# Optimization experiments

Hardware: AMD Instinct MI355X
Metric: run time of the kernel (lower is better)

## Reference

```python
import jax, jax.numpy as jnp
import numpy as np


def setup_inputs() -> dict:
    key = jax.random.key(0)
    ks = jax.random.split(key, 8)
    B, A = 2048, 64
    STATE, ACT = 5, 4
    d_in = STATE + ACT  # 9
    x = jax.random.normal(ks[0], (B, STATE), dtype=jnp.float32)
    actions = jax.random.normal(ks[1], (A, ACT), dtype=jnp.float32)
    def lin(k, fin, fout):
        return jax.random.normal(k, (fin, fout), dtype=jnp.float32) / np.sqrt(fin)
    W1 = lin(ks[2], d_in, 128); b1 = jnp.zeros((128,), jnp.float32)
    W2 = lin(ks[3], 128, 1024); b2 = jnp.zeros((1024,), jnp.float32)
    W3 = lin(ks[4], 1024, 1024); b3 = jnp.zeros((1024,), jnp.float32)
    W4 = lin(ks[5], 1024, 128); b4 = jnp.zeros((128,), jnp.float32)
    W5 = lin(ks[6], 128, 1); b5 = jnp.zeros((1,), jnp.float32)
    return {"x": x, "actions": actions,
            "W1": W1, "b1": b1, "W2": W2, "b2": b2, "W3": W3, "b3": b3,
            "W4": W4, "b4": b4, "W5": W5, "b5": b5}


def reference(x, actions, W1, b1, W2, b2, W3, b3, W4, b4, W5, b5):
    # x: [B,5] states; actions: [A,4] candidate actions.
    # Equivalent to the original's per-sample per-action loop: evaluate the
    # 5-layer Tanh MLP on concat(state, action) for every (sample, action) pair.
    B = x.shape[0]
    A = actions.shape[0]
    s = jnp.broadcast_to(x[:, None, :], (B, A, x.shape[1]))
    a = jnp.broadcast_to(actions[None, :, :], (B, A, actions.shape[1]))
    inp = jnp.concatenate([s, a], axis=-1)  # [B,A,9]
    h = jnp.tanh(inp @ W1 + b1)
    h = jnp.tanh(h @ W2 + b2)
    h = jnp.tanh(h @ W3 + b3)
    h = jnp.tanh(h @ W4 + b4)
    values = (h @ W5 + b5)[..., 0]  # [B,A]
    best = jnp.argmax(values, axis=1)  # [B]
    max_value_action = actions[best]  # [B,4]
    return (max_value_action, values)
```

## Files before the change

kernel.cpp:

```cpp
#include <hip/hip_runtime.h>
#include <hip/hip_bf16.h>
#include <math.h>


typedef short bf16x8 __attribute__((ext_vector_type(8)));
typedef float f32x4 __attribute__((ext_vector_type(4)));
typedef float f32x16 __attribute__((ext_vector_type(16)));

__device__ __host__ inline unsigned short f2bf(float f) {
    union { float f; unsigned u; } v; v.f = f;
    unsigned r = v.u + 0x7fff + ((v.u >> 16) & 1);
    return (unsigned short)(r >> 16);
}
__device__ inline unsigned short cvt_bf16(float f) {
    __hip_bfloat16 h = __float2bfloat16(f);
    return *reinterpret_cast<unsigned short*>(&h);
}
__device__ inline float bf2f(unsigned short b) {
    union { unsigned u; float f; } v; v.u = ((unsigned)b) << 16;
    return v.f;
}
__device__ inline float fast_tanh(float x) {
    float e = __expf(2.0f * x);
    return 1.0f - 2.0f * __builtin_amdgcn_rcpf(e + 1.0f);
}

#define DELTA 0.025f
#define ITEM_CAP 16384

struct WLE { unsigned s, base, nc, pad; };

#define HSWZ(row, b) ((b) ^ (((row) & 15) << 4))

__global__ __launch_bounds__(256) void pack_all(
    const float* __restrict__ W2, const float* __restrict__ W3, const float* __restrict__ W4,
    unsigned short* __restrict__ W2p, unsigned short* __restrict__ W3p,
    unsigned short* __restrict__ W4p, unsigned* __restrict__ cnts)
{
    int tid = blockIdx.x * 256 + threadIdx.x;
    if (tid < 2) cnts[tid] = 0u;
    int blob = tid >> 6, lane = tid & 63;
    if (blob >= 2560) return;
    bf16x8 v;
    if (blob < 256) {
        int nt = blob >> 2, kt = blob & 3;
        int n = nt * 16 + (lane & 15);
        int kbase = kt * 32 + ((lane >> 4) & 3) * 8;
        #pragma unroll
        for (int e = 0; e < 8; ++e) v[e] = (short)f2bf(W2[(size_t)(kbase + e) * 1024 + n]);
        *(bf16x8*)&W2p[(size_t)blob * 512 + lane * 8] = v;
    } else if (blob < 2304) {
        int lb = blob - 256;
        int nt = lb >> 6, kt = lb & 63;
        int n = nt * 32 + (lane & 31);
        int kbase = kt * 16 + (lane >> 5) * 8;
        #pragma unroll
        for (int e = 0; e < 8; ++e) v[e] = (short)f2bf(W3[(size_t)(kbase + e) * 1024 + n]);
        *(bf16x8*)&W3p[(size_t)lb * 512 + lane * 8] = v;
    } else {
        int lb = blob - 2304;
        int nt = lb >> 5, kt = lb & 31;
        int n = nt * 16 + (lane & 15);
        int kbase = kt * 32 + ((lane >> 4) & 3) * 8;
        #pragma unroll
        for (int e = 0; e < 8; ++e) v[e] = (short)f2bf(W4[(size_t)(kbase + e) * 128 + n]);
        *(bf16x8*)&W4p[(size_t)lb * 512 + lane * 8] = v;
    }
}

__global__ __launch_bounds__(1024, 4) void qnet_mfma(
    const float* __restrict__ x, const float* __restrict__ actions,
    const float* __restrict__ W1, const float* __restrict__ b1,
    const float* __restrict__ b2, const float* __restrict__ b3,
    const float* __restrict__ b4,
    const float* __restrict__ W5, const float* __restrict__ b5,
    const unsigned short* __restrict__ W2p,
    const unsigned short* __restrict__ W3p,
    const unsigned short* __restrict__ W4p,
    float* __restrict__ values, float* __restrict__ out_actions,
    unsigned* __restrict__ cnts, WLE* __restrict__ wl,
    unsigned* __restrict__ items)
{
    __shared__ unsigned short h2b[2][64 * 256];
    __shared__ unsigned short hc[64 * 128];

    const int t = threadIdx.x;
    const int lane = t & 63;
    const int wave = t >> 6;
    const int grp = (wave >> 2) & 1;
    const int p0 = blockIdx.x * 64;
    const int l15 = lane & 15;
    const int kb16 = (lane >> 4) * 16;
    const int kb32 = (lane >> 5) * 16;

    {
        int r = t >> 4;
        int c0 = (t & 15) * 8;
        const float* xs = &x[blockIdx.x * 5];
        const float* as = &actions[r * 4];
        float in[9] = { xs[0], xs[1], xs[2], xs[3], xs[4], as[0], as[1], as[2], as[3] };
        #pragma unroll
        for (int j = 0; j < 8; ++j) {
            int c = c0 + j;
            float acc = b1[c];
            #pragma unroll
            for (int k = 0; k < 9; ++k) acc += in[k] * W1[k * 128 + c];
            *(unsigned short*)((char*)hc + r * 256 + HSWZ(r, c * 2)) = cvt_bf16(fast_tanh(acc));
        }
    }
    __syncthreads();

    auto layer2_chunk = [&](int c, int buf) {
        const int nT = c * 16 + wave;
        const float bv = b2[nT * 16 + l15];
        char* bufp = (char*)&h2b[buf][0];
        const int lcb = (wave * 16 + l15) * 2;
        #pragma unroll 1
        for (int rt = 0; rt < 4; ++rt) {
            f32x4 acc = (f32x4){ bv, bv, bv, bv };
            const int row = rt * 16 + l15;
            #pragma unroll
            for (int ks = 0; ks < 4; ++ks) {
                bf16x8 b = *(const bf16x8*)((const char*)W2p + (nT * 4 + ks) * 1024 + lane * 16);
                bf16x8 a = *(const bf16x8*)((const char*)hc + row * 256 + HSWZ(row, ks * 64 + kb16));
                acc = __builtin_amdgcn_mfma_f32_16x16x32_bf16(a, b, acc, 0, 0, 0);
            }
            #pragma unroll
            for (int rr = 0; rr < 4; ++rr) {
                int m = rt * 16 + (lane >> 4) * 4 + rr;
                *(unsigned short*)(bufp + m * 512 + HSWZ(m, lcb)) = cvt_bf16(fast_tanh(acc[rr]));
            }
        }
    };

    f32x16 a00, a01, a10, a11;
    {
        float bv0 = b3[wave * 64 + (lane & 31)];
        float bv1 = b3[wave * 64 + 32 + (lane & 31)];
        #pragma unroll
        for (int i = 0; i < 16; ++i) { a00[i] = bv0; a10[i] = bv0; a01[i] = bv1; a11[i] = bv1; }
    }
    const int r0 = lane & 31, r1 = 32 + (lane & 31);

    auto l3_step = [&](int c) {
        const char* bufp = (const char*)&h2b[c & 1][0];
        const char* bb = (const char*)W3p + (wave * 128 + c * 16) * 1024 + lane * 16;
        __builtin_amdgcn_s_setprio(1);
        #pragma unroll 2
        for (int kt = 0; kt < 16; ++kt) {
            bf16x8 A0 = *(const bf16x8*)(bufp + r0 * 512 + HSWZ(r0, kt * 32 + kb32));
            bf16x8 A1 = *(const bf16x8*)(bufp + r1 * 512 + HSWZ(r1, kt * 32 + kb32));
            bf16x8 B0 = *(const bf16x8*)(bb + kt * 1024);
            bf16x8 B1 = *(const bf16x8*)(bb + 65536 + kt * 1024);
            a00 = __builtin_amdgcn_mfma_f32_32x32x16_bf16(A0, B0, a00, 0, 0, 0);
            a10 = __builtin_amdgcn_mfma_f32_32x32x16_bf16(A1, B0, a10, 0, 0, 0);
            a01 = __builtin_amdgcn_mfma_f32_32x32x16_bf16(A0, B1, a01, 0, 0, 0);
            a11 = __builtin_amdgcn_mfma_f32_32x32x16_bf16(A1, B1, a11, 0, 0, 0);
        }
        __builtin_amdgcn_s_setprio(0);
    };

    layer2_chunk(0, 0);
    __syncthreads();

    for (int c = 0; c < 4; ++c) {
        if (grp == 0) {
            if (c < 3) layer2_chunk(c + 1, (c + 1) & 1);
            l3_step(c);
        } else {
            l3_step(c);
            if (c < 3) layer2_chunk(c + 1, (c + 1) & 1);
        }
        __syncthreads();
    }

    char* stage = (char*)&h2b[0][0];
    const int ct = wave & 7, rtp = wave >> 3;
    const int c0b = (wave * 64 + (lane & 31)) * 2;
    const float bv4 = b4[ct * 16 + l15];

    #pragma unroll
    for (int h = 0; h < 2; ++h) {
        #pragma unroll
        for (int r = 0; r < 16; ++r) {
            int row = (r & 3) + 8 * (r >> 2) + 4 * (lane >> 5);
            float vlo = h ? a10[r] : a00[r];
            float vhi = h ? a11[r] : a01[r];
            *(unsigned short*)(stage + row * 2048 + HSWZ(row, c0b)) = cvt_bf16(fast_tanh(vlo));
            *(unsigned short*)(stage + row * 2048 + HSWZ(row, c0b + 64)) = cvt_bf16(fast_tanh(vhi));
        }
        __syncthreads();
        f32x4 acc4 = (f32x4){ bv4, bv4, bv4, bv4 };
        const int rowL = rtp * 16 + l15;
        #pragma unroll 4
        for (int k32 = 0; k32 < 32; ++k32) {
            bf16x8 B = *(const bf16x8*)((const char*)W4p + (ct * 32 + k32) * 1024 + lane * 16);
            bf16x8 a = *(const bf16x8*)(stage + rowL * 2048 + HSWZ(rowL, k32 * 64 + kb16));
            acc4 = __builtin_amdgcn_mfma_f32_16x16x32_bf16(a, B, acc4, 0, 0, 0);
        }
        int n = ct * 16 + l15;
        #pragma unroll
        for (int rr = 0; rr < 4; ++rr) {
            int m = h * 32 + rtp * 16 + (lane >> 4) * 4 + rr;
            *(unsigned short*)((char*)hc + m * 256 + HSWZ(m, n * 2)) = cvt_bf16(fast_tanh(acc4[rr]));
        }
        __syncthreads();
    }

    float* vbuf = (float*)&h2b[0][0];
    {
        int r = t >> 4, g = t & 15;
        float part = 0.0f;
        #pragma unroll
        for (int j = 0; j < 8; ++j) {
            int cidx = g * 8 + j;
            unsigned short hb = *(const unsigned short*)((const char*)hc + r * 256 + HSWZ(r, cidx * 2));
            part += bf2f(hb) * W5[cidx];
        }
        part += __shfl_down(part, 8);
        part += __shfl_down(part, 4);
        part += __shfl_down(part, 2);
        part += __shfl_down(part, 1);
        if (g == 0) {
            float val = part + b5[0];
            values[p0 + r] = val;
            vbuf[r] = val;
        }
    }
    __syncthreads();

    if (t < 64) {
        float myv = vbuf[t];
        float v = myv; int idx = t;
        #pragma unroll
        for (int off = 32; off; off >>= 1) {
            float ov = __shfl_down(v, off);
            int oi = __shfl_down(idx, off);
            if (ov > v || (ov == v && oi < idx)) { v = ov; idx = oi; }
        }
        float vm = __shfl(v, 0);
        int best = __shfl(idx, 0);
        if (t < 4) out_actions[blockIdx.x * 4 + t] = actions[best * 4 + t];
        unsigned long long mask = __ballot(myv >= vm - DELTA);
        int nc = __popcll(mask);
        if (nc > 1) {
            unsigned base = 0;
            if (t == 0) base = atomicAdd(&cnts[1], (unsigned)nc);
            base = (unsigned)__shfl((int)base, 0);
            if (base + (unsigned)nc <= (unsigned)ITEM_CAP) {
                if (t == 0) {
                    unsigned slot = atomicAdd(&cnts[0], 1u);
                    wl[slot].s = blockIdx.x; wl[slot].base = base; wl[slot].nc = (unsigned)nc;
                }
                if (myv >= vm - DELTA) {
                    int rank = __popcll(mask & ((1ull << t) - 1ull));
                    items[base + rank] = ((unsigned)blockIdx.x << 6) | (unsigned)t;
                }
            }
        }
    }
}

__global__ __launch_bounds__(256) void fixup_eval(
    const float* __restrict__ x, const float* __restrict__ actions,
    const float* __restrict__ W1, const float* __restrict__ b1,
    const float* __restrict__ W2, const float* __restrict__ b2,
    const float* __restrict__ W3, const float* __restrict__ b3,
    const float* __restrict__ W4, const float* __restrict__ b4,
    const float* __restrict__ W5, const float* __restrict__ b5,
    const unsigned* __restrict__ cnts, const unsigned* __restrict__ items,
    float* __restrict__ vexact)
{
    __shared__ float h1s[8][128];
    __shared__ float h2s[8][1024];
    __shared__ float h3s[8][1024];
    __shared__ float h4s[8][128];
    __shared__ float xin[8][5];
    __shared__ float ain[8][4];

    const int t = threadIdx.x;
    int n = (int)cnts[1]; if (n > ITEM_CAP) n = ITEM_CAP;
    int nb = (n + 7) >> 3;
    for (int b = blockIdx.x; b < nb; b += gridDim.x) {
        if (t < 8) {
            int idx = b * 8 + t;
            unsigned it = items[(idx < n) ? idx : (b * 8)];
            int s = (int)((it >> 6) & 2047), a = (int)(it & 63);
            #pragma unroll
            for (int k = 0; k < 5; ++k) xin[t][k] = x[s * 5 + k];
            #pragma unroll
            for (int k = 0; k < 4; ++k) ain[t][k] = actions[a * 4 + k];
        }
        __syncthreads();
        {
            int r = t >> 5, cb = (t & 31) * 4;
            #pragma unroll
            for (int j = 0; j < 4; ++j) {
                int c = cb + j;
                float acc = b1[c];
                #pragma unroll
                for (int k = 0; k < 5; ++k) acc += xin[r][k] * W1[k * 128 + c];
                #pragma unroll
                for (int k = 0; k < 4; ++k) acc += ain[r][k] * W1[(5 + k) * 128 + c];
                h1s[r][c] = tanhf(acc);
            }
        }
        __syncthreads();
        {
            int cb = t * 4;
            float acc[8][4];
            float4 bv = *(const float4*)&b2[cb];
            #pragma unroll
            for (int r = 0; r < 8; ++r) { acc[r][0]=bv.x; acc[r][1]=bv.y; acc[r][2]=bv.z; acc[r][3]=bv.w; }
            for (int k = 0; k < 128; ++k) {
                float4 w = *(const float4*)&W2[k * 1024 + cb];
                #pragma unroll
                for (int r = 0; r < 8; ++r) {
                    float hv = h1s[r][k];
                    acc[r][0] += hv * w.x; acc[r][1] += hv * w.y;
                    acc[r][2] += hv * w.z; acc[r][3] += hv * w.w;
                }
            }
            #pragma unroll
            for (int r = 0; r < 8; ++r) {
                h2s[r][cb+0] = tanhf(acc[r][0]); h2s[r][cb+1] = tanhf(acc[r][1]);
                h2s[r][cb+2] = tanhf(acc[r][2]); h2s[r][cb+3] = tanhf(acc[r][3]);
            }
        }
        __syncthreads();
        {
            int cb = t * 4;
            float acc[8][4];
            float4 bv = *(const float4*)&b3[cb];
            #pragma unroll
            for (int r = 0; r < 8; ++r) { acc[r][0]=bv.x; acc[r][1]=bv.y; acc[r][2]=bv.z; acc[r][3]=bv.w; }
            for (int k = 0; k < 1024; ++k) {
                float4 w = *(const float4*)&W3[k * 1024 + cb];
                #pragma unroll
                for (int r = 0; r < 8; ++r) {
                    float hv = h2s[r][k];
                    acc[r][0] += hv * w.x; acc[r][1] += hv * w.y;
                    acc[r][2] += hv * w.z; acc[r][3] += hv * w.w;
                }
            }
            #pragma unroll
            for (int r = 0; r < 8; ++r) {
                h3s[r][cb+0] = tanhf(acc[r][0]); h3s[r][cb+1] = tanhf(acc[r][1]);
                h3s[r][cb+2] = tanhf(acc[r][2]); h3s[r][cb+3] = tanhf(acc[r][3]);
            }
        }
        __syncthreads();
        {
            int r = t >> 5, cb = (t & 31) * 4;
            float acc[4];
            float4 bv = *(const float4*)&b4[cb];
            acc[0]=bv.x; acc[1]=bv.y; acc[2]=bv.z; acc[3]=bv.w;
            for (int k = 0; k < 1024; ++k) {
                float4 w = *(const float4*)&W4[k * 128 + cb];
                float hv = h3s[r][k];
                acc[0] += hv * w.x; acc[1] += hv * w.y; acc[2] += hv * w.z; acc[3] += hv * w.w;
            }
            h4s[r][cb+0] = tanhf(acc[0]); h4s[r][cb+1] = tanhf(acc[1]);
            h4s[r][cb+2] = tanhf(acc[2]); h4s[r][cb+3] = tanhf(acc[3]);
        }
        __syncthreads();
        if (t < 8) {
            float acc = b5[0];
            for (int k = 0; k < 128; ++k) acc += h4s[t][k] * W5[k];
            int idx = b * 8 + t;
            if (idx < n) vexact[idx] = acc;
        }
        __syncthreads();
    }
}

__global__ __launch_bounds__(256) void finalize_argmax(
    const unsigned* __restrict__ cnts, const WLE* __restrict__ wl,
    const unsigned* __restrict__ items, const float* __restrict__ vexact,
    const float* __restrict__ actions, float* __restrict__ out_actions)
{
    int gw = (blockIdx.x * 256 + threadIdx.x) >> 6;
    int lane = threadIdx.x & 63;
    int nwl = (int)cnts[0]; if (nwl > 2048) nwl = 2048;
    if (gw >= nwl) return;
    unsigned s = wl[gw].s, base = wl[gw].base, nc = wl[gw].nc;
    float v = (lane < (int)nc) ? vexact[base + lane] : -3.0e38f;
    int idx = lane;
    #pragma unroll
    for (int off = 32; off; off >>= 1) {
        float ov = __shfl_down(v, off);
        int oi = __shfl_down(idx, off);
        if (ov > v || (ov == v && oi < idx)) { v = ov; idx = oi; }
    }
    int i0 = __shfl(idx, 0);
    int a = (int)(items[base + i0] & 63);
    if (lane < 4) out_actions[s * 4 + lane] = actions[a * 4 + lane];
}

#define TR 16
__global__ __launch_bounds__(256) void qnet_fused(
    const float* __restrict__ x, const float* __restrict__ actions,
    const float* __restrict__ W1, const float* __restrict__ b1,
    const float* __restrict__ W2, const float* __restrict__ b2,
    const float* __restrict__ W3, const float* __restrict__ b3,
    const float* __restrict__ W4, const float* __restrict__ b4,
    const float* __restrict__ W5, const float* __restrict__ b5,
    float* __restrict__ values)
{
    __shared__ float h_small[TR][128];
    __shared__ float hA[TR][1024];
    __shared__ float hB[TR][1024];
    const int t = threadIdx.x;
    const int p0 = blockIdx.x * TR;
    for (int i = t; i < TR * 128; i += 256) {
        int r = i >> 7, c = i & 127;
        int p = p0 + r;
        int bidx = p >> 6, aidx = p & 63;
        float acc = b1[c];
        for (int k = 0; k < 5; ++k) acc += x[bidx * 5 + k] * W1[k * 128 + c];
        for (int k = 0; k < 4; ++k) acc += actions[aidx * 4 + k] * W1[(5 + k) * 128 + c];
        h_small[r][c] = tanhf(acc);
    }
    __syncthreads();
    {
        const int c0 = t * 4;
        float4 bias = *(const float4*)&b2[c0];
        float acc[TR][4];
        for (int r = 0; r < TR; ++r) { acc[r][0]=bias.x; acc[r][1]=bias.y; acc[r][2]=bias.z; acc[r][3]=bias.w; }
        for (int k = 0; k < 128; k += 4) {
            float4 w0 = *(const float4*)&W2[(k+0)*1024+c0];
            float4 w1 = *(const float4*)&W2[(k+1)*1024+c0];
            float4 w2 = *(const float4*)&W2[(k+2)*1024+c0];
            float4 w3 = *(const float4*)&W2[(k+3)*1024+c0];
            for (int r = 0; r < TR; ++r) {
                float4 hv = *(const float4*)&h_small[r][k];
                acc[r][0] += hv.x*w0.x + hv.y*w1.x + hv.z*w2.x + hv.w*w3.x;
                acc[r][1] += hv.x*w0.y + hv.y*w1.y + hv.z*w2.y + hv.w*w3.y;
                acc[r][2] += hv.x*w0.z + hv.y*w1.z + hv.z*w2.z + hv.w*w3.z;
                acc[r][3] += hv.x*w0.w + hv.y*w1.w + hv.z*w2.w + hv.w*w3.w;
            }
        }
        for (int r = 0; r < TR; ++r) {
            hA[r][c0+0]=tanhf(acc[r][0]); hA[r][c0+1]=tanhf(acc[r][1]);
            hA[r][c0+2]=tanhf(acc[r][2]); hA[r][c0+3]=tanhf(acc[r][3]);
        }
    }
    __syncthreads();
    {
        const int c0 = t * 4;
        float4 bias = *(const float4*)&b3[c0];
        float acc[TR][4];
        for (int r = 0; r < TR; ++r) { acc[r][0]=bias.x; acc[r][1]=bias.y; acc[r][2]=bias.z; acc[r][3]=bias.w; }
        for (int k = 0; k < 1024; k += 4) {
            float4 w0 = *(const float4*)&W3[(k+0)*1024+c0];
            float4 w1 = *(const float4*)&W3[(k+1)*1024+c0];
            float4 w2 = *(const float4*)&W3[(k+2)*1024+c0];
            float4 w3 = *(const float4*)&W3[(k+3)*1024+c0];
            for (int r = 0; r < TR; ++r) {
                float4 hv = *(const float4*)&hA[r][k];
                acc[r][0] += hv.x*w0.x + hv.y*w1.x + hv.z*w2.x + hv.w*w3.x;
                acc[r][1] += hv.x*w0.y + hv.y*w1.y + hv.z*w2.y + hv.w*w3.y;
                acc[r][2] += hv.x*w0.z + hv.y*w1.z + hv.z*w2.z + hv.w*w3.z;
                acc[r][3] += hv.x*w0.w + hv.y*w1.w + hv.z*w2.w + hv.w*w3.w;
            }
        }
        for (int r = 0; r < TR; ++r) {
            hB[r][c0+0]=tanhf(acc[r][0]); hB[r][c0+1]=tanhf(acc[r][1]);
            hB[r][c0+2]=tanhf(acc[r][2]); hB[r][c0+3]=tanhf(acc[r][3]);
        }
    }
    __syncthreads();
    {
        const int c = t & 127;
        const int rh = t >> 7;
        float acc[8];
        float bias = b4[c];
        for (int r = 0; r < 8; ++r) acc[r] = bias;
        for (int k = 0; k < 1024; k += 4) {
            float w0 = W4[(k+0)*128+c], w1 = W4[(k+1)*128+c];
            float w2 = W4[(k+2)*128+c], w3 = W4[(k+3)*128+c];
            for (int r = 0; r < 8; ++r) {
                float4 hv = *(const float4*)&hB[rh*8+r][k];
                acc[r] += hv.x*w0 + hv.y*w1 + hv.z*w2 + hv.w*w3;
            }
        }
        for (int r = 0; r < 8; ++r) h_small[rh*8+r][c] = tanhf(acc[r]);
    }
    __syncthreads();
    if (t < TR) {
        float acc = b5[0];
        for (int k = 0; k < 128; k += 4) {
            float4 hv = *(const float4*)&h_small[t][k];
            float4 wv = *(const float4*)&W5[k];
            acc += hv.x*wv.x + hv.y*wv.y + hv.z*wv.z + hv.w*wv.w;
        }
        values[p0 + t] = acc;
    }
}

__global__ __launch_bounds__(256) void argmax_gather(
    const float* __restrict__ values, const float* __restrict__ actions,
    float* __restrict__ out_actions)
{
    const int wave = threadIdx.x >> 6;
    const int lane = threadIdx.x & 63;
    const int state = blockIdx.x * (blockDim.x >> 6) + wave;
    float v = values[state * 64 + lane];
    int idx = lane;
    for (int off = 32; off; off >>= 1) {
        float ov = __shfl_down(v, off);
        int oi = __shfl_down(idx, off);
        if (ov > v || (ov == v && oi < idx)) { v = ov; idx = oi; }
    }
    idx = __shfl(idx, 0);
    if (lane < 4) out_actions[state * 4 + lane] = actions[idx * 4 + lane];
}

extern "C" void kernel_launch(void* const* d_in, const int* in_sizes, int n_in,
                              void* d_out, int out_size, void* d_ws, size_t ws_size,
                              hipStream_t stream) {
    const float* x       = (const float*)d_in[0];
    const float* actions = (const float*)d_in[1];
    const float* W1 = (const float*)d_in[2];  const float* b1 = (const float*)d_in[3];
    const float* W2 = (const float*)d_in[4];  const float* b2 = (const float*)d_in[5];
    const float* W3 = (const float*)d_in[6];  const float* b3 = (const float*)d_in[7];
    const float* W4 = (const float*)d_in[8];  const float* b4 = (const float*)d_in[9];
    const float* W5 = (const float*)d_in[10]; const float* b5 = (const float*)d_in[11];

    float* out_actions = (float*)d_out;
    float* values      = (float*)d_out + 2048 * 4;

    const size_t nW2 = 128 * 1024, nW3 = 1024 * 1024, nW4 = 1024 * 128;
    const size_t wbytes = (nW2 + nW3 + nW4) * sizeof(unsigned short);
    const size_t need = wbytes + 16 + 2048 * sizeof(WLE) + ITEM_CAP * 4 + ITEM_CAP * 4;

    if (ws_size >= need) {
        unsigned short* W2p = (unsigned short*)d_ws;
        unsigned short* W3p = W2p + nW2;
        unsigned short* W4p = W3p + nW3;
        char* p = (char*)d_ws + wbytes;
        unsigned* cnts = (unsigned*)p;                 p += 16;
        WLE* wl = (WLE*)p;                             p += 2048 * sizeof(WLE);
        unsigned* items = (unsigned*)p;                p += ITEM_CAP * 4;
        float* vexact = (float*)p;

        pack_all<<<640, 256, 0, stream>>>(W2, W3, W4, W2p, W3p, W4p, cnts);
        qnet_mfma<<<2048, 1024, 0, stream>>>(x, actions, W1, b1, b2, b3, b4, W5, b5,
                                             W2p, W3p, W4p, values, out_actions,
                                             cnts, wl, items);
        fixup_eval<<<512, 256, 0, stream>>>(x, actions, W1, b1, W2, b2, W3, b3,
                                            W4, b4, W5, b5, cnts, items, vexact);
        finalize_argmax<<<512, 256, 0, stream>>>(cnts, wl, items, vexact,
                                                 actions, out_actions);
    } else {
        qnet_fused<<<2048 * 64 / TR, 256, 0, stream>>>(x, actions, W1, b1, W2, b2, W3, b3,
                                                       W4, b4, W5, b5, values);
        argmax_gather<<<2048 / 4, 256, 0, stream>>>(values, actions, out_actions);
    }
}
```

Baseline: 622.0 us.

## Replace chunked layer2/layer3 ping-pong pipeline with full h2 staging in LDS

Drops the four-chunk double-buffered schedule, in which wave groups alternated between computing layer-2 chunks and layer-3 partial products. Layer 2 is now computed in full into a 64x1024 bf16 LDS buffer, with A fragments held in registers and reused across four output tiles. Layer 3 then runs one uninterrupted 64-step K loop. Layer 4 is done in a single pass with two accumulators instead of two halves separated by barriers. This removes several barriers and the setprio juggling, but it gives up the overlap between layers 2 and 3 and raises LDS use to about 144KB per block, which could limit occupancy.

```diff
diff --git a/kernel.cpp b/kernel.cpp
--- a/kernel.cpp
+++ b/kernel.cpp
@@ -81,15 +81,13 @@
     unsigned* __restrict__ cnts, WLE* __restrict__ wl,
     unsigned* __restrict__ items)
 {
-    __shared__ unsigned short h2b[2][64 * 256];
+    __shared__ unsigned short h2[64 * 1024];
     __shared__ unsigned short hc[64 * 128];
 
     const int t = threadIdx.x;
     const int lane = t & 63;
     const int wave = t >> 6;
-    const int grp = (wave >> 2) & 1;
     const int p0 = blockIdx.x * 64;
-    const int l15 = lane & 15;
     const int kb16 = (lane >> 4) * 16;
     const int kb32 = (lane >> 5) * 16;
 
@@ -110,28 +108,41 @@
     }
     __syncthreads();
 
-    auto layer2_chunk = [&](int c, int buf) {
-        const int nT = c * 16 + wave;
-        const float bv = b2[nT * 16 + l15];
-        char* bufp = (char*)&h2b[buf][0];
-        const int lcb = (wave * 16 + l15) * 2;
-        #pragma unroll 1
-        for (int rt = 0; rt < 4; ++rt) {
-            f32x4 acc = (f32x4){ bv, bv, bv, bv };
-            const int row = rt * 16 + l15;
+    {
+        bf16x8 Af[4][4];
+        #pragma unroll
+        for (int rt = 0; rt < 4; ++rt)
             #pragma unroll
             for (int ks = 0; ks < 4; ++ks) {
-                bf16x8 b = *(const bf16x8*)((const char*)W2p + (nT * 4 + ks) * 1024 + lane * 16);
-                bf16x8 a = *(const bf16x8*)((const char*)hc + row * 256 + HSWZ(row, ks * 64 + kb16));
-                acc = __builtin_amdgcn_mfma_f32_16x16x32_bf16(a, b, acc, 0, 0, 0);
-            }
+                int row = rt * 16 + (lane & 15);
+                Af[rt][ks] = *(const bf16x8*)((const char*)hc + row * 256 + HSWZ(row, ks * 64 + kb16));
+            }
+        #pragma unroll
+        for (int j = 0; j < 4; ++j) {
+            int nT = wave * 4 + j;
+            float bv = b2[nT * 16 + (lane & 15)];
+            f32x4 acc0 = (f32x4){ bv, bv, bv, bv };
+            f32x4 acc1 = acc0, acc2 = acc0, acc3v = acc0;
+            #pragma unroll
+            for (int ks = 0; ks < 4; ++ks) {
+                bf16x8 b = *(const bf16x8*)&W2p[((size_t)(nT * 4 + ks)) * 512 + lane * 8];
+                acc0 = __builtin_amdgcn_mfma_f32_16x16x32_bf16(Af[0][ks], b, acc0, 0, 0, 0);
+                acc1 = __builtin_amdgcn_mfma_f32_16x16x32_bf16(Af[1][ks], b, acc1, 0, 0, 0);
+                acc2 = __builtin_amdgcn_mfma_f32_16x16x32_bf16(Af[2][ks], b, acc2, 0, 0, 0);
+                acc3v = __builtin_amdgcn_mfma_f32_16x16x32_bf16(Af[3][ks], b, acc3v, 0, 0, 0);
+            }
+            int n = nT * 16 + (lane & 15);
             #pragma unroll
             for (int rr = 0; rr < 4; ++rr) {
-                int m = rt * 16 + (lane >> 4) * 4 + rr;
-                *(unsigned short*)(bufp + m * 512 + HSWZ(m, lcb)) = cvt_bf16(fast_tanh(acc[rr]));
-            }
-        }
-    };
+                int m0 = (lane >> 4) * 4 + rr;
+                *(unsigned short*)((char*)h2 + (m0 +  0) * 2048 + HSWZ(m0 +  0, n * 2)) = cvt_bf16(fast_tanh(acc0[rr]));
+                *(unsigned short*)((char*)h2 + (m0 + 16) * 2048 + HSWZ(m0 + 16, n * 2)) = cvt_bf16(fast_tanh(acc1[rr]));
+                *(unsigned short*)((char*)h2 + (m0 + 32) * 2048 + HSWZ(m0 + 32, n * 2)) = cvt_bf16(fast_tanh(acc2[rr]));
+                *(unsigned short*)((char*)h2 + (m0 + 48) * 2048 + HSWZ(m0 + 48, n * 2)) = cvt_bf16(fast_tanh(acc3v[rr]));
+            }
+        }
+    }
+    __syncthreads();
 
     f32x16 a00, a01, a10, a11;
     {
@@ -141,73 +152,63 @@
         for (int i = 0; i < 16; ++i) { a00[i] = bv0; a10[i] = bv0; a01[i] = bv1; a11[i] = bv1; }
     }
     const int r0 = lane & 31, r1 = 32 + (lane & 31);
-
-    auto l3_step = [&](int c) {
-        const char* bufp = (const char*)&h2b[c & 1][0];
-        const char* bb = (const char*)W3p + (wave * 128 + c * 16) * 1024 + lane * 16;
-        __builtin_amdgcn_s_setprio(1);
+    {
+        const unsigned short* bbase = &W3p[((size_t)(wave * 2) * 64) * 512 + lane * 8];
         #pragma unroll 2
-        for (int kt = 0; kt < 16; ++kt) {
-            bf16x8 A0 = *(const bf16x8*)(bufp + r0 * 512 + HSWZ(r0, kt * 32 + kb32));
-            bf16x8 A1 = *(const bf16x8*)(bufp + r1 * 512 + HSWZ(r1, kt * 32 + kb32));
-            bf16x8 B0 = *(const bf16x8*)(bb + kt * 1024);
-            bf16x8 B1 = *(const bf16x8*)(bb + 65536 + kt * 1024);
+        for (int kt = 0; kt < 64; ++kt) {
+            bf16x8 A0 = *(const bf16x8*)((const char*)h2 + r0 * 2048 + HSWZ(r0, kt * 32 + kb32));
+            bf16x8 A1 = *(const bf16x8*)((const char*)h2 + r1 * 2048 + HSWZ(r1, kt * 32 + kb32));
+            bf16x8 B0 = *(const bf16x8*)(bbase + (size_t)kt * 512);
+            bf16x8 B1 = *(const bf16x8*)(bbase + (size_t)(64 + kt) * 512);
             a00 = __builtin_amdgcn_mfma_f32_32x32x16_bf16(A0, B0, a00, 0, 0, 0);
             a10 = __builtin_amdgcn_mfma_f32_32x32x16_bf16(A1, B0, a10, 0, 0, 0);
             a01 = __builtin_amdgcn_mfma_f32_32x32x16_bf16(A0, B1, a01, 0, 0, 0);
             a11 = __builtin_amdgcn_mfma_f32_32x32x16_bf16(A1, B1, a11, 0, 0, 0);
         }
-        __builtin_amdgcn_s_setprio(0);
-    };
-
-    layer2_chunk(0, 0);
-    __syncthreads();
-
-    for (int c = 0; c < 4; ++c) {
-        if (grp == 0) {
-            if (c < 3) layer2_chunk(c + 1, (c + 1) & 1);
-            l3_step(c);
-        } else {
-            l3_step(c);
-            if (c < 3) layer2_chunk(c + 1, (c + 1) & 1);
-        }
-        __syncthreads();
-    }
-
-    char* stage = (char*)&h2b[0][0];
-    const int ct = wave & 7, rtp = wave >> 3;
-    const int c0b = (wave * 64 + (lane & 31)) * 2;
-    const float bv4 = b4[ct * 16 + l15];
-
-    #pragma unroll
-    for (int h = 0; h < 2; ++h) {
+    }
+    __syncthreads();
+
+    {
+        int c0l = wave * 64 + (lane & 31);
         #pragma unroll
         for (int r = 0; r < 16; ++r) {
             int row = (r & 3) + 8 * (r >> 2) + 4 * (lane >> 5);
-            float vlo = h ? a10[r] : a00[r];
-            float vhi = h ? a11[r] : a01[r];
-            *(unsigned short*)(stage + row * 2048 + HSWZ(row, c0b)) = cvt_bf16(fast_tanh(vlo));
-            *(unsigned short*)(stage + row * 2048 + HSWZ(row, c0b + 64)) = cvt_bf16(fast_tanh(vhi));
-        }
-        __syncthreads();
-        f32x4 acc4 = (f32x4){ bv4, bv4, bv4, bv4 };
-        const int rowL = rtp * 16 + l15;
+            int rowB = row + 32;
+            *(unsigned short*)((char*)h2 + row  * 2048 + HSWZ(row,  c0l * 2)) = cvt_bf16(fast_tanh(a00[r]));
+            *(unsigned short*)((char*)h2 + rowB * 2048 + HSWZ(rowB, c0l * 2)) = cvt_bf16(fast_tanh(a10[r]));
+            *(unsigned short*)((char*)h2 + row  * 2048 + HSWZ(row,  (c0l + 32) * 2)) = cvt_bf16(fast_tanh(a01[r]));
+            *(unsigned short*)((char*)h2 + rowB * 2048 + HSWZ(rowB, (c0l + 32) * 2)) = cvt_bf16(fast_tanh(a11[r]));
+        }
+    }
+    __syncthreads();
+
+    {
+        const int ct = wave & 7, rtp = wave >> 3;
+        const int rowA = rtp * 32 + (lane & 15);
+        const int rowB = rowA + 16;
+        float bv = b4[ct * 16 + (lane & 15)];
+        f32x4 acc4a = (f32x4){ bv, bv, bv, bv };
+        f32x4 acc4b = acc4a;
         #pragma unroll 4
         for (int k32 = 0; k32 < 32; ++k32) {
-            bf16x8 B = *(const bf16x8*)((const char*)W4p + (ct * 32 + k32) * 1024 + lane * 16);
-            bf16x8 a = *(const bf16x8*)(stage + rowL * 2048 + HSWZ(rowL, k32 * 64 + kb16));
-            acc4 = __builtin_amdgcn_mfma_f32_16x16x32_bf16(a, B, acc4, 0, 0, 0);
-        }
-        int n = ct * 16 + l15;
+            bf16x8 B = *(const bf16x8*)&W4p[((size_t)(ct * 32 + k32)) * 512 + lane * 8];
+            bf16x8 aA = *(const bf16x8*)((const char*)h2 + rowA * 2048 + HSWZ(rowA, k32 * 64 + kb16));
+            bf16x8 aB = *(const bf16x8*)((const char*)h2 + rowB * 2048 + HSWZ(rowB, k32 * 64 + kb16));
+            acc4a = __builtin_amdgcn_mfma_f32_16x16x32_bf16(aA, B, acc4a, 0, 0, 0);
+            acc4b = __builtin_amdgcn_mfma_f32_16x16x32_bf16(aB, B, acc4b, 0, 0, 0);
+        }
+        int n = ct * 16 + (lane & 15);
         #pragma unroll
         for (int rr = 0; rr < 4; ++rr) {
-            int m = h * 32 + rtp * 16 + (lane >> 4) * 4 + rr;
-            *(unsigned short*)((char*)hc + m * 256 + HSWZ(m, n * 2)) = cvt_bf16(fast_tanh(acc4[rr]));
-        }
-        __syncthreads();
-    }
-
-    float* vbuf = (float*)&h2b[0][0];
+            int mA = rtp * 32 + (lane >> 4) * 4 + rr;
+            int mB = mA + 16;
+            *(unsigned short*)((char*)hc + mA * 256 + HSWZ(mA, n * 2)) = cvt_bf16(fast_tanh(acc4a[rr]));
+            *(unsigned short*)((char*)hc + mB * 256 + HSWZ(mB, n * 2)) = cvt_bf16(fast_tanh(acc4b[rr]));
+        }
+    }
+    __syncthreads();
+
+    float* vbuf = (float*)&h2[0];
     {
         int r = t >> 4, g = t & 15;
         float part = 0.0f;
```

Result: faster. 594.5 us (-4.4%).
